# Kernel tuning notes

Measured on AMD Instinct MI355X. Metric: run time of the kernel, lower is better.

The kernel has to match this reference:

```python
import jax, jax.numpy as jnp
import numpy as np

N_COMPRESS = 2048
N_EXPAND_QK = 1024
N_EXPAND_V = 1024
TOPK_C, TOPK_QK, TOPK_V = 8, 4, 6


def _topk_sparsify(w, k):
    # top-k along last dim, scatter back, renormalize (matches torch scatter_ path)
    vals, idx = jax.lax.top_k(w, k)                      # [B,k]
    rows = jnp.arange(w.shape[0])[:, None]
    sparse = jnp.zeros_like(w).at[rows, idx].set(vals)   # [B,N]
    return sparse / (sparse.sum(axis=-1, keepdims=True) + 1e-8)


def setup_inputs() -> dict:
    key = jax.random.key(0)
    k0, k1, k2, k3 = jax.random.split(key, 4)
    B, S, D, DS = 4, 4096, 2048, 64
    total = N_COMPRESS + N_EXPAND_QK + N_EXPAND_V
    return {
        "x": jax.random.normal(k0, (B, S, D), jnp.float32),
        "importance": jax.random.uniform(k1, (B, S), jnp.float32),
        "W": jax.random.normal(k2, (D, DS), jnp.float32) * 0.02,
        "b": jnp.zeros((DS,), jnp.float32),
        "neuron_emb": jax.random.normal(k3, (total, DS), jnp.float32) * 0.02,
    }


def reference(x, importance, W, b, neuron_emb):
    # projection (dropout is identity in eval mode)
    h = x @ W + b                                             # [B,S,ds]
    # cosine logits against unit-norm neuron embeddings
    emb_n = neuron_emb / jnp.linalg.norm(neuron_emb, axis=-1, keepdims=True)
    all_logits = jnp.einsum('bsd,nd->bsn', h, emb_n)          # [B,S,total]
    lC = all_logits[..., :N_COMPRESS]
    lQK = all_logits[..., N_COMPRESS:N_COMPRESS + N_EXPAND_QK]
    lV = all_logits[..., N_COMPRESS + N_EXPAND_QK:]
    pC = jax.nn.softmax(lC, axis=-1)
    pQK = jax.nn.softmax(lQK, axis=-1)   # expand_Q and expand_K share the slice (eval: identical)
    pV = jax.nn.softmax(lV, axis=-1)
    # importance-weighted pooling to per-batch dense routing weights
    dC = jnp.einsum('bs,bsn->bn', importance, pC)
    dQK = jnp.einsum('bs,bsn->bn', importance, pQK)
    dV = jnp.einsum('bs,bsn->bn', importance, pV)
    wC = _topk_sparsify(dC, TOPK_C)
    wQ = _topk_sparsify(dQK, TOPK_QK)
    wK = _topk_sparsify(dQK, TOPK_QK)
    wV = _topk_sparsify(dV, TOPK_V)
    # concat the four routing-weight outputs: [B, 2048+1024+1024+1024]
    return jnp.concatenate([wC, wQ, wK, wV], axis=-1)
```

## Files before the change

### kernel.cpp

```cpp
#include <hip/hip_runtime.h>
#include <math.h>

#define D_IN   2048

typedef __bf16 bf16x8 __attribute__((ext_vector_type(8)));
typedef __bf16 bf16x4 __attribute__((ext_vector_type(4)));
typedef float  f32x4  __attribute__((ext_vector_type(4)));
typedef float  f32x16 __attribute__((ext_vector_type(16)));

__global__ __launch_bounds__(256) void k_prepe(const float* __restrict__ emb,
                                               __bf16* __restrict__ e_hi,
                                               __bf16* __restrict__ e_lo) {
    int gid  = blockIdx.x * 256 + threadIdx.x;
    int row  = gid >> 6;
    int lane = gid & 63;
    float v  = emb[row * 64 + lane];
    float ss = v * v;
#pragma unroll
    for (int m = 32; m >= 1; m >>= 1) ss += __shfl_xor(ss, m);
    float nv = v / sqrtf(ss);
    __bf16 hb = (__bf16)nv;
    e_hi[row * 64 + lane] = hb;
    e_lo[row * 64 + lane] = (__bf16)(nv - (float)hb);
}

__global__ __launch_bounds__(256) void k_prepw(const float* __restrict__ W,
                                               __bf16* __restrict__ wt_hi,
                                               __bf16* __restrict__ wt_lo) {
    int gid = blockIdx.x * 256 + threadIdx.x;
    int c   = gid >> 11;
    int k   = gid & 2047;
    float v = W[k * 64 + c];
    __bf16 hb = (__bf16)v;
    wt_hi[c * 2048 + k] = hb;
    wt_lo[c * 2048 + k] = (__bf16)(v - (float)hb);
}

__global__ __launch_bounds__(256, 2) void k_hgemm_mfma(
        const float* __restrict__ x,
        const __bf16* __restrict__ wt_hi, const __bf16* __restrict__ wt_lo,
        float* __restrict__ pc) {
    int t     = threadIdx.x;
    int wave  = t >> 6;
    int lane  = t & 63;
    int l15   = lane & 15;
    int kg    = lane >> 4;
    int rblk  = blockIdx.x & 255;
    int kh    = blockIdx.x >> 8;
    int row0  = rblk * 64 + wave * 16;
    int kbase = kh * 1024;

    const float*  xp    = x + (size_t)(row0 + l15) * D_IN + kbase + kg * 8;
    const __bf16* bh_p0 = wt_hi + (size_t)(0  + l15) * D_IN + kbase + kg * 8;
    const __bf16* bh_p1 = bh_p0 + 16 * D_IN;
    const __bf16* bh_p2 = bh_p0 + 32 * D_IN;
    const __bf16* bh_p3 = bh_p0 + 48 * D_IN;
    const __bf16* bl_p0 = wt_lo + (size_t)(0  + l15) * D_IN + kbase + kg * 8;
    const __bf16* bl_p1 = bl_p0 + 16 * D_IN;
    const __bf16* bl_p2 = bl_p0 + 32 * D_IN;
    const __bf16* bl_p3 = bl_p0 + 48 * D_IN;

    f32x4 acc0 = {0.f,0.f,0.f,0.f}, acc1 = {0.f,0.f,0.f,0.f};
    f32x4 acc2 = {0.f,0.f,0.f,0.f}, acc3 = {0.f,0.f,0.f,0.f};

    float4 e_a0, e_a1, o_a0, o_a1;
    bf16x8 e_bh0, e_bh1, e_bh2, e_bh3, e_bl0, e_bl1, e_bl2, e_bl3;
    bf16x8 o_bh0, o_bh1, o_bh2, o_bh3, o_bl0, o_bl1, o_bl2, o_bl3;

#define LDA(S, KO) { S##_a0 = *(const float4*)(xp + (KO)); \
                     S##_a1 = *(const float4*)(xp + (KO) + 4); }
#define LDB(S, KO) { S##_bh0 = *(const bf16x8*)(bh_p0 + (KO)); \
                     S##_bh1 = *(const bf16x8*)(bh_p1 + (KO)); \
                     S##_bh2 = *(const bf16x8*)(bh_p2 + (KO)); \
                     S##_bh3 = *(const bf16x8*)(bh_p3 + (KO)); \
                     S##_bl0 = *(const bf16x8*)(bl_p0 + (KO)); \
                     S##_bl1 = *(const bf16x8*)(bl_p1 + (KO)); \
                     S##_bl2 = *(const bf16x8*)(bl_p2 + (KO)); \
                     S##_bl3 = *(const bf16x8*)(bl_p3 + (KO)); }
#define COMP(S) { \
    float av[8] = {S##_a0.x, S##_a0.y, S##_a0.z, S##_a0.w, \
                   S##_a1.x, S##_a1.y, S##_a1.z, S##_a1.w}; \
    bf16x8 ah, al; \
    _Pragma("unroll") \
    for (int j = 0; j < 8; ++j) { \
        __bf16 hb = (__bf16)av[j]; ah[j] = hb; \
        al[j] = (__bf16)(av[j] - (float)hb); \
    } \
    acc0 = __builtin_amdgcn_mfma_f32_16x16x32_bf16(ah, S##_bh0, acc0, 0, 0, 0); \
    acc1 = __builtin_amdgcn_mfma_f32_16x16x32_bf16(ah, S##_bh1, acc1, 0, 0, 0); \
    acc2 = __builtin_amdgcn_mfma_f32_16x16x32_bf16(ah, S##_bh2, acc2, 0, 0, 0); \
    acc3 = __builtin_amdgcn_mfma_f32_16x16x32_bf16(ah, S##_bh3, acc3, 0, 0, 0); \
    acc0 = __builtin_amdgcn_mfma_f32_16x16x32_bf16(ah, S##_bl0, acc0, 0, 0, 0); \
    acc1 = __builtin_amdgcn_mfma_f32_16x16x32_bf16(ah, S##_bl1, acc1, 0, 0, 0); \
    acc2 = __builtin_amdgcn_mfma_f32_16x16x32_bf16(ah, S##_bl2, acc2, 0, 0, 0); \
    acc3 = __builtin_amdgcn_mfma_f32_16x16x32_bf16(ah, S##_bl3, acc3, 0, 0, 0); \
    acc0 = __builtin_amdgcn_mfma_f32_16x16x32_bf16(al, S##_bh0, acc0, 0, 0, 0); \
    acc1 = __builtin_amdgcn_mfma_f32_16x16x32_bf16(al, S##_bh1, acc1, 0, 0, 0); \
    acc2 = __builtin_amdgcn_mfma_f32_16x16x32_bf16(al, S##_bh2, acc2, 0, 0, 0); \
    acc3 = __builtin_amdgcn_mfma_f32_16x16x32_bf16(al, S##_bh3, acc3, 0, 0, 0); }

    LDA(e, 0) LDB(e, 0)
#pragma unroll
    for (int it = 0; it < 30; it += 2) {
        LDA(o, (it + 1) * 32) LDB(o, (it + 1) * 32)
        COMP(e)
        LDA(e, (it + 2) * 32) LDB(e, (it + 2) * 32)
        COMP(o)
    }
    LDA(o, 31 * 32) LDB(o, 31 * 32)
    COMP(e)
    COMP(o)
#undef LDA
#undef LDB
#undef COMP

    float* dst = pc + (size_t)kh * 16384 * 64 + (size_t)(row0 + kg * 4) * 64 + l15;
#pragma unroll
    for (int r = 0; r < 4; ++r) {
        dst[(size_t)r * 64 + 0]  = acc0[r];
        dst[(size_t)r * 64 + 16] = acc1[r];
        dst[(size_t)r * 64 + 32] = acc2[r];
        dst[(size_t)r * 64 + 48] = acc3[r];
    }
}

__global__ __launch_bounds__(256) void k_hfix(const float* __restrict__ pc,
                                              const float* __restrict__ bias,
                                              __bf16* __restrict__ h_hi,
                                              __bf16* __restrict__ h_lo) {
    int gid = blockIdx.x * 256 + threadIdx.x;
    int i4  = gid * 4;
    float4 p0 = *(const float4*)(pc + i4);
    float4 p1 = *(const float4*)(pc + (size_t)16384 * 64 + i4);
    float4 bb = *(const float4*)(bias + (i4 & 63));
    float hv[4] = {p0.x + p1.x + bb.x, p0.y + p1.y + bb.y,
                   p0.z + p1.z + bb.z, p0.w + p1.w + bb.w};
    bf16x4 vhi, vlo;
#pragma unroll
    for (int j = 0; j < 4; ++j) {
        __bf16 hb = (__bf16)hv[j];
        vhi[j] = hb;
        vlo[j] = (__bf16)(hv[j] - (float)hb);
    }
    *(bf16x4*)&h_hi[i4] = vhi;
    *(bf16x4*)&h_lo[i4] = vlo;
}

__global__ __launch_bounds__(512, 2) void k_logits(
        const __bf16* __restrict__ h_hi, const __bf16* __restrict__ h_lo,
        const __bf16* __restrict__ e_hi, const __bf16* __restrict__ e_lo,
        const float* __restrict__ imp, float* __restrict__ partials) {
    __shared__ float zs[8][2][16];
    int t    = threadIdx.x;
    int wave = t >> 6;
    int lane = t & 63;
    int l31  = lane & 31;
    int h5   = lane >> 5;
    int wr   = wave >> 2;
    int wc   = wave & 3;
    int row0 = blockIdx.x * 64 + wr * 32;

    bf16x8 a_hi[4], a_lo[4];
    {
        const __bf16* hp = h_hi + (size_t)(row0 + l31) * 64 + h5 * 8;
        const __bf16* lp = h_lo + (size_t)(row0 + l31) * 64 + h5 * 8;
#pragma unroll
        for (int ks = 0; ks < 4; ++ks) {
            a_hi[ks] = *(const bf16x8*)(hp + ks * 16);
            a_lo[ks] = *(const bf16x8*)(lp + ks * 16);
        }
    }
    float impv[16];
#pragma unroll
    for (int r = 0; r < 16; ++r)
        impv[r] = imp[row0 + (r & 3) + 8 * (r >> 2) + 4 * h5];

    int b    = blockIdx.x >> 6;
    int slot = (blockIdx.x & 63) * 2 + wr;
    float* pbase = partials + ((size_t)(b * 128 + slot)) * 4096;

    const int segB[4] = {0, 2048, 3072, 4096};
    for (int sg = 0; sg < 3; ++sg) {
        float zacc[16];
#pragma unroll
        for (int r = 0; r < 16; ++r) zacc[r] = 0.f;
        for (int nb = segB[sg]; nb < segB[sg + 1]; nb += 128) {
            const __bf16* ep = e_hi + (size_t)(nb + wc * 32 + l31) * 64 + h5 * 8;
            const __bf16* lp = e_lo + (size_t)(nb + wc * 32 + l31) * 64 + h5 * 8;
            bf16x8 b_hi[4], b_lo[4];
#pragma unroll
            for (int ks = 0; ks < 4; ++ks) {
                b_hi[ks] = *(const bf16x8*)(ep + ks * 16);
                b_lo[ks] = *(const bf16x8*)(lp + ks * 16);
            }
            f32x16 acc = {0.f,0.f,0.f,0.f,0.f,0.f,0.f,0.f,
                          0.f,0.f,0.f,0.f,0.f,0.f,0.f,0.f};
#pragma unroll
            for (int ks = 0; ks < 4; ++ks) {
                acc = __builtin_amdgcn_mfma_f32_32x32x16_bf16(a_hi[ks], b_hi[ks], acc, 0, 0, 0);
                acc = __builtin_amdgcn_mfma_f32_32x32x16_bf16(a_hi[ks], b_lo[ks], acc, 0, 0, 0);
                acc = __builtin_amdgcn_mfma_f32_32x32x16_bf16(a_lo[ks], b_hi[ks], acc, 0, 0, 0);
            }
#pragma unroll
            for (int r = 0; r < 16; ++r) zacc[r] += __expf(acc[r]);
        }
#pragma unroll
        for (int r = 0; r < 16; ++r) {
            float z = zacc[r];
#pragma unroll
            for (int m = 1; m < 32; m <<= 1) z += __shfl_xor(z, m);
            zacc[r] = z;
        }
        if (l31 == 0) {
#pragma unroll
            for (int r = 0; r < 16; ++r) zs[wave][h5][r] = zacc[r];
        }
        __syncthreads();
        float coef[16];
#pragma unroll
        for (int r = 0; r < 16; ++r) {
            float z = zs[wr * 4 + 0][h5][r] + zs[wr * 4 + 1][h5][r] +
                      zs[wr * 4 + 2][h5][r] + zs[wr * 4 + 3][h5][r];
            coef[r] = impv[r] / z;
        }
        __syncthreads();
        for (int nb = segB[sg]; nb < segB[sg + 1]; nb += 128) {
            const __bf16* ep = e_hi + (size_t)(nb + wc * 32 + l31) * 64 + h5 * 8;
            const __bf16* lp = e_lo + (size_t)(nb + wc * 32 + l31) * 64 + h5 * 8;
            bf16x8 b_hi[4], b_lo[4];
#pragma unroll
            for (int ks = 0; ks < 4; ++ks) {
                b_hi[ks] = *(const bf16x8*)(ep + ks * 16);
                b_lo[ks] = *(const bf16x8*)(lp + ks * 16);
            }
            f32x16 acc = {0.f,0.f,0.f,0.f,0.f,0.f,0.f,0.f,
                          0.f,0.f,0.f,0.f,0.f,0.f,0.f,0.f};
#pragma unroll
            for (int ks = 0; ks < 4; ++ks) {
                acc = __builtin_amdgcn_mfma_f32_32x32x16_bf16(a_hi[ks], b_hi[ks], acc, 0, 0, 0);
                acc = __builtin_amdgcn_mfma_f32_32x32x16_bf16(a_hi[ks], b_lo[ks], acc, 0, 0, 0);
                acc = __builtin_amdgcn_mfma_f32_32x32x16_bf16(a_lo[ks], b_hi[ks], acc, 0, 0, 0);
            }
            float s = 0.f;
#pragma unroll
            for (int r = 0; r < 16; ++r) s += coef[r] * __expf(acc[r]);
            s += __shfl_xor(s, 32);
            if (h5 == 0) pbase[nb + wc * 32 + l31] = s;
        }
    }
}

__global__ __launch_bounds__(256) void k_reduce(const float* __restrict__ partials,
                                                float* __restrict__ dacc) {
    int blk = blockIdx.x;
    int b   = blk >> 4;
    int n   = (blk & 15) * 256 + threadIdx.x;
    const float* p = partials + (size_t)b * 128 * 4096 + n;
    float s0 = 0.f, s1 = 0.f, s2 = 0.f, s3 = 0.f;
#pragma unroll 4
    for (int s = 0; s < 128; s += 4) {
        s0 += p[(size_t)(s + 0) * 4096];
        s1 += p[(size_t)(s + 1) * 4096];
        s2 += p[(size_t)(s + 2) * 4096];
        s3 += p[(size_t)(s + 3) * 4096];
    }
    dacc[b * 4096 + n] = (s0 + s1) + (s2 + s3);
}

__global__ __launch_bounds__(256) void k_topk(const float* __restrict__ dacc,
                                              float* __restrict__ out) {
    __shared__ float dv[2048];
    __shared__ float redv[4];
    __shared__ int   redi[4];
    __shared__ float selv[8];
    __shared__ int   seli[8];
    int blk = blockIdx.x;
    int b   = blk / 3;
    int sg  = blk - 3 * b;
    int t   = threadIdx.x;
    const int segStart[3] = {0, 2048, 3072};
    const int segLen[3]   = {2048, 1024, 1024};
    const int segK[3]     = {8, 4, 6};
    const int segOut[3]   = {0, 2048, 4096};
    int st = segStart[sg], len = segLen[sg], kk = segK[sg];
    for (int n = t; n < len; n += 256) dv[n] = dacc[b * 4096 + st + n];
    __syncthreads();
    for (int it = 0; it < kk; ++it) {
        float bv = -3.0e38f;
        int   bi = 1 << 30;
        for (int n = t; n < len; n += 256) {
            float v = dv[n];
            if (v > bv) { bv = v; bi = n; }
        }
#pragma unroll
        for (int m = 1; m < 64; m <<= 1) {
            float ov = __shfl_xor(bv, m);
            int   oi = __shfl_xor(bi, m);
            if (ov > bv || (ov == bv && oi < bi)) { bv = ov; bi = oi; }
        }
        if ((t & 63) == 0) { redv[t >> 6] = bv; redi[t >> 6] = bi; }
        __syncthreads();
        if (t == 0) {
            for (int w = 1; w < 4; ++w)
                if (redv[w] > bv || (redv[w] == bv && redi[w] < bi)) {
                    bv = redv[w]; bi = redi[w];
                }
            selv[it] = bv;
            seli[it] = bi;
            dv[bi] = -3.4e38f;
        }
        __syncthreads();
    }
    float sum = 0.f;
    for (int it = 0; it < kk; ++it) sum += selv[it];
    float inv = 1.0f / (sum + 1e-8f);
    for (int n = t; n < len; n += 256) {
        float v = 0.0f;
        for (int it = 0; it < kk; ++it)
            if (seli[it] == n) v = selv[it] * inv;
        out[b * 5120 + segOut[sg] + n] = v;
        if (sg == 1) out[b * 5120 + 3072 + n] = v;
    }
}

extern "C" void kernel_launch(void* const* d_in, const int* in_sizes, int n_in,
                              void* d_out, int out_size, void* d_ws, size_t ws_size,
                              hipStream_t stream) {
    (void)in_sizes; (void)n_in; (void)out_size; (void)ws_size;
    const float* x    = (const float*)d_in[0];
    const float* imp  = (const float*)d_in[1];
    const float* W    = (const float*)d_in[2];
    const float* bias = (const float*)d_in[3];
    const float* emb  = (const float*)d_in[4];
    float* out = (float*)d_out;

    char* w = (char*)d_ws;
    __bf16* e_hi  = (__bf16*)w;  w += (size_t)4096 * 64 * 2;
    __bf16* e_lo  = (__bf16*)w;  w += (size_t)4096 * 64 * 2;
    __bf16* h_hi  = (__bf16*)w;  w += (size_t)16384 * 64 * 2;
    __bf16* h_lo  = (__bf16*)w;  w += (size_t)16384 * 64 * 2;
    __bf16* wt_hi = (__bf16*)w;  w += (size_t)64 * 2048 * 2;
    __bf16* wt_lo = (__bf16*)w;  w += (size_t)64 * 2048 * 2;
    float*  pc    = (float*)w;
    float*  partials = (float*)w; w += (size_t)4 * 128 * 4096 * 4;
    float*  dacc  = (float*)w;   w += (size_t)4 * 4096 * 4;

    hipLaunchKernelGGL(k_prepe,      dim3(1024), dim3(256), 0, stream, emb, e_hi, e_lo);
    hipLaunchKernelGGL(k_prepw,      dim3(512),  dim3(256), 0, stream, W, wt_hi, wt_lo);
    hipLaunchKernelGGL(k_hgemm_mfma, dim3(512),  dim3(256), 0, stream, x, wt_hi, wt_lo, pc);
    hipLaunchKernelGGL(k_hfix,       dim3(1024), dim3(256), 0, stream, pc, bias, h_hi, h_lo);
    hipLaunchKernelGGL(k_logits,     dim3(256),  dim3(512), 0, stream, h_hi, h_lo,
                       e_hi, e_lo, imp, partials);
    hipLaunchKernelGGL(k_reduce,     dim3(64),   dim3(256), 0, stream, partials, dacc);
    hipLaunchKernelGGL(k_topk,       dim3(12),   dim3(256), 0, stream, dacc, out);
}
```

Baseline: 402.8 us.

## Give each logits block 32 rows across 8 waves and split MFMA accumulators

The logits kernel now assigns 32 rows per block with all 8 waves covering different neuron columns, instead of 64 rows split into two 4-wave groups. The grid doubles to 512 blocks, and the launch bound allows 4 blocks per CU. The three-term bf16 split MFMA chain now uses two independent accumulators to shorten the dependency chain, and B fragments are loaded inside the ks loop to reduce register pressure. The aim is more occupancy and parallelism. The cost is that each e fragment is reloaded by twice as many blocks, plus a cross-8-wave shared-memory reduction for the softmax denominators.

```diff
diff --git a/kernel.cpp b/kernel.cpp
--- a/kernel.cpp
+++ b/kernel.cpp
@@ -146,7 +146,7 @@
     *(bf16x4*)&h_lo[i4] = vlo;
 }
 
-__global__ __launch_bounds__(512, 2) void k_logits(
+__global__ __launch_bounds__(512, 4) void k_logits(
         const __bf16* __restrict__ h_hi, const __bf16* __restrict__ h_lo,
         const __bf16* __restrict__ e_hi, const __bf16* __restrict__ e_lo,
         const float* __restrict__ imp, float* __restrict__ partials) {
@@ -156,9 +156,7 @@
     int lane = t & 63;
     int l31  = lane & 31;
     int h5   = lane >> 5;
-    int wr   = wave >> 2;
-    int wc   = wave & 3;
-    int row0 = blockIdx.x * 64 + wr * 32;
+    int row0 = blockIdx.x * 32;
 
     bf16x8 a_hi[4], a_lo[4];
     {
@@ -170,13 +168,9 @@
             a_lo[ks] = *(const bf16x8*)(lp + ks * 16);
         }
     }
-    float impv[16];
-#pragma unroll
-    for (int r = 0; r < 16; ++r)
-        impv[r] = imp[row0 + (r & 3) + 8 * (r >> 2) + 4 * h5];
-
-    int b    = blockIdx.x >> 6;
-    int slot = (blockIdx.x & 63) * 2 + wr;
+
+    int b    = blockIdx.x >> 7;
+    int slot = blockIdx.x & 127;
     float* pbase = partials + ((size_t)(b * 128 + slot)) * 4096;
 
     const int segB[4] = {0, 2048, 3072, 4096};
@@ -184,25 +178,22 @@
         float zacc[16];
 #pragma unroll
         for (int r = 0; r < 16; ++r) zacc[r] = 0.f;
-        for (int nb = segB[sg]; nb < segB[sg + 1]; nb += 128) {
-            const __bf16* ep = e_hi + (size_t)(nb + wc * 32 + l31) * 64 + h5 * 8;
-            const __bf16* lp = e_lo + (size_t)(nb + wc * 32 + l31) * 64 + h5 * 8;
-            bf16x8 b_hi[4], b_lo[4];
+        for (int nb = segB[sg]; nb < segB[sg + 1]; nb += 256) {
+            const __bf16* ep = e_hi + (size_t)(nb + wave * 32 + l31) * 64 + h5 * 8;
+            const __bf16* lp = e_lo + (size_t)(nb + wave * 32 + l31) * 64 + h5 * 8;
+            f32x16 ac1 = {0.f,0.f,0.f,0.f,0.f,0.f,0.f,0.f,
+                          0.f,0.f,0.f,0.f,0.f,0.f,0.f,0.f};
+            f32x16 ac2 = ac1;
 #pragma unroll
             for (int ks = 0; ks < 4; ++ks) {
-                b_hi[ks] = *(const bf16x8*)(ep + ks * 16);
-                b_lo[ks] = *(const bf16x8*)(lp + ks * 16);
+                bf16x8 bh = *(const bf16x8*)(ep + ks * 16);
+                bf16x8 bl = *(const bf16x8*)(lp + ks * 16);
+                ac1 = __builtin_amdgcn_mfma_f32_32x32x16_bf16(a_hi[ks], bh, ac1, 0, 0, 0);
+                ac2 = __builtin_amdgcn_mfma_f32_32x32x16_bf16(a_lo[ks], bh, ac2, 0, 0, 0);
+                ac1 = __builtin_amdgcn_mfma_f32_32x32x16_bf16(a_hi[ks], bl, ac1, 0, 0, 0);
             }
-            f32x16 acc = {0.f,0.f,0.f,0.f,0.f,0.f,0.f,0.f,
-                          0.f,0.f,0.f,0.f,0.f,0.f,0.f,0.f};
-#pragma unroll
-            for (int ks = 0; ks < 4; ++ks) {
-                acc = __builtin_amdgcn_mfma_f32_32x32x16_bf16(a_hi[ks], b_hi[ks], acc, 0, 0, 0);
-                acc = __builtin_amdgcn_mfma_f32_32x32x16_bf16(a_hi[ks], b_lo[ks], acc, 0, 0, 0);
-                acc = __builtin_amdgcn_mfma_f32_32x32x16_bf16(a_lo[ks], b_hi[ks], acc, 0, 0, 0);
-            }
-#pragma unroll
-            for (int r = 0; r < 16; ++r) zacc[r] += __expf(acc[r]);
+#pragma unroll
+            for (int r = 0; r < 16; ++r) zacc[r] += __expf(ac1[r] + ac2[r]);
         }
 #pragma unroll
         for (int r = 0; r < 16; ++r) {
@@ -219,33 +210,31 @@
         float coef[16];
 #pragma unroll
         for (int r = 0; r < 16; ++r) {
-            float z = zs[wr * 4 + 0][h5][r] + zs[wr * 4 + 1][h5][r] +
-                      zs[wr * 4 + 2][h5][r] + zs[wr * 4 + 3][h5][r];
-            coef[r] = impv[r] / z;
+            float z = 0.f;
+#pragma unroll
+            for (int w = 0; w < 8; ++w) z += zs[w][h5][r];
+            coef[r] = imp[row0 + (r & 3) + 8 * (r >> 2) + 4 * h5] / z;
         }
         __syncthreads();
-        for (int nb = segB[sg]; nb < segB[sg + 1]; nb += 128) {
-            const __bf16* ep = e_hi + (size_t)(nb + wc * 32 + l31) * 64 + h5 * 8;
-            const __bf16* lp = e_lo + (size_t)(nb + wc * 32 + l31) * 64 + h5 * 8;
-            bf16x8 b_hi[4], b_lo[4];
+        for (int nb = segB[sg]; nb < segB[sg + 1]; nb += 256) {
+            const __bf16* ep = e_hi + (size_t)(nb + wave * 32 + l31) * 64 + h5 * 8;
+            const __bf16* lp = e_lo + (size_t)(nb + wave * 32 + l31) * 64 + h5 * 8;
+            f32x16 ac1 = {0.f,0.f,0.f,0.f,0.f,0.f,0.f,0.f,
+                          0.f,0.f,0.f,0.f,0.f,0.f,0.f,0.f};
+            f32x16 ac2 = ac1;
 #pragma unroll
             for (int ks = 0; ks < 4; ++ks) {
-                b_hi[ks] = *(const bf16x8*)(ep + ks * 16);
-                b_lo[ks] = *(const bf16x8*)(lp + ks * 16);
-            }
-            f32x16 acc = {0.f,0.f,0.f,0.f,0.f,0.f,0.f,0.f,
-                          0.f,0.f,0.f,0.f,0.f,0.f,0.f,0.f};
-#pragma unroll
-            for (int ks = 0; ks < 4; ++ks) {
-                acc = __builtin_amdgcn_mfma_f32_32x32x16_bf16(a_hi[ks], b_hi[ks], acc, 0, 0, 0);
-                acc = __builtin_amdgcn_mfma_f32_32x32x16_bf16(a_hi[ks], b_lo[ks], acc, 0, 0, 0);
-                acc = __builtin_amdgcn_mfma_f32_32x32x16_bf16(a_lo[ks], b_hi[ks], acc, 0, 0, 0);
+                bf16x8 bh = *(const bf16x8*)(ep + ks * 16);
+                bf16x8 bl = *(const bf16x8*)(lp + ks * 16);
+                ac1 = __builtin_amdgcn_mfma_f32_32x32x16_bf16(a_hi[ks], bh, ac1, 0, 0, 0);
+                ac2 = __builtin_amdgcn_mfma_f32_32x32x16_bf16(a_lo[ks], bh, ac2, 0, 0, 0);
+                ac1 = __builtin_amdgcn_mfma_f32_32x32x16_bf16(a_hi[ks], bl, ac1, 0, 0, 0);
             }
             float s = 0.f;
 #pragma unroll
-            for (int r = 0; r < 16; ++r) s += coef[r] * __expf(acc[r]);
+            for (int r = 0; r < 16; ++r) s += coef[r] * __expf(ac1[r] + ac2[r]);
             s += __shfl_xor(s, 32);
-            if (h5 == 0) pbase[nb + wc * 32 + l31] = s;
+            if (h5 == 0) pbase[nb + wave * 32 + l31] = s;
         }
     }
 }
@@ -349,7 +338,7 @@
     hipLaunchKernelGGL(k_prepw,      dim3(512),  dim3(256), 0, stream, W, wt_hi, wt_lo);
     hipLaunchKernelGGL(k_hgemm_mfma, dim3(512),  dim3(256), 0, stream, x, wt_hi, wt_lo, pc);
     hipLaunchKernelGGL(k_hfix,       dim3(1024), dim3(256), 0, stream, pc, bias, h_hi, h_lo);
-    hipLaunchKernelGGL(k_logits,     dim3(256),  dim3(512), 0, stream, h_hi, h_lo,
+    hipLaunchKernelGGL(k_logits,     dim3(512),  dim3(512), 0, stream, h_hi, h_lo,
                        e_hi, e_lo, imp, partials);
     hipLaunchKernelGGL(k_reduce,     dim3(64),   dim3(256), 0, stream, partials, dacc);
     hipLaunchKernelGGL(k_topk,       dim3(12),   dim3(256), 0, stream, dacc, out);
```

Measured after the change: 447.3 us. 1.11x slower.
